# Optimization experiments

Hardware: AMD Instinct MI355X
Metric: run time of the kernel (lower is better)

## Reference

```python
import jax, jax.numpy as jnp
import numpy as np

N_NODES = 100000
N_EDGES = 1600000
IN_F = 128
OUT_F = 64
BN_EPS = 1e-5


def setup_inputs() -> dict:
    key = jax.random.key(0)
    ks = jax.random.split(key, 6)
    feature = jax.random.normal(ks[0], (N_NODES, IN_F), dtype=jnp.float32)
    src = jax.random.randint(ks[1], (N_EDGES,), 0, N_NODES, dtype=jnp.int32)
    dst = jax.random.randint(ks[2], (N_EDGES,), 0, N_NODES, dtype=jnp.int32)
    W = jax.random.normal(ks[3], (IN_F, OUT_F), dtype=jnp.float32) * 0.05
    b = jnp.zeros((OUT_F,), dtype=jnp.float32)
    res_W = jax.random.normal(ks[4], (IN_F, OUT_F), dtype=jnp.float32) * 0.05
    res_b = jnp.zeros((OUT_F,), dtype=jnp.float32)
    gamma = jnp.ones((OUT_F,), dtype=jnp.float32)
    beta = jnp.zeros((OUT_F,), dtype=jnp.float32)
    return {"feature": feature, "src": src, "dst": dst, "W": W, "b": b,
            "res_W": res_W, "res_b": res_b, "gamma": gamma, "beta": beta,
            "idx": 0}


def _gcn_layer(feature, src, dst, W, b, res_W, res_b, gamma, beta):
    n = feature.shape[0]
    ones = jnp.ones_like(src, dtype=feature.dtype)
    # DGL norm='both': src-side uses out-degree, dst-side uses in-degree,
    # degrees clamped to min 1 (allow_zero_in_degree=True).
    out_deg = jax.ops.segment_sum(ones, src, num_segments=n)
    in_deg = jax.ops.segment_sum(ones, dst, num_segments=n)
    norm_src = jax.lax.rsqrt(jnp.maximum(out_deg, 1.0))  # [N]
    norm_dst = jax.lax.rsqrt(jnp.maximum(in_deg, 1.0))   # [N]

    # in_feats (128) > out_feats (64): DGL multiplies by W before aggregation.
    h = (feature * norm_src[:, None]) @ W                 # [N, OUT_F]
    agg = jax.ops.segment_sum(h[src], dst, num_segments=n)  # [N, OUT_F]
    conv = jax.nn.relu(agg * norm_dst[:, None] + b)

    # residual connection: activation(Linear(feature))
    res = jax.nn.relu(feature @ res_W + res_b)
    y = conv + res

    # BatchNorm1d (training mode, biased variance)
    mean = jnp.mean(y, axis=0)
    var = jnp.mean(jnp.square(y - mean), axis=0)
    y = (y - mean) * jax.lax.rsqrt(var + BN_EPS) * gamma + beta
    return y


def reference(feature, src, dst, W, b, res_W, res_b, gamma, beta, idx):
    # idx == 0 -> dropout branch is skipped (eval-deterministic reference)
    return _gcn_layer(feature, src, dst, W, b, res_W, res_b, gamma, beta)
```

## Files before the change

kernel.cpp:

```cpp
#include <hip/hip_runtime.h>
#include <hip/hip_fp16.h>

#define NCOL 64
#define KDIM 128
#define NB 512
#define CH 2048

typedef short bf16x8 __attribute__((ext_vector_type(8)));
typedef float f32x4 __attribute__((ext_vector_type(4)));
typedef float f32x2 __attribute__((ext_vector_type(2)));

__device__ __forceinline__ unsigned short f2bf(float f) {
    unsigned int u = __float_as_uint(f);
    return (unsigned short)((u + 0x7fffu + ((u >> 16) & 1u)) >> 16);
}

__global__ __launch_bounds__(256) void coarse_hist(const int* __restrict__ src,
                                                   const int* __restrict__ dst,
                                                   int* __restrict__ outcnt,
                                                   int* __restrict__ bcnt, int E) {
    __shared__ int lh[NB];
    int tid = threadIdx.x;
    for (int i = tid; i < NB; i += 256) lh[i] = 0;
    __syncthreads();
    int i = blockIdx.x * blockDim.x + tid;
    int stride = gridDim.x * blockDim.x;
    for (int e = i; e < E; e += stride) {
        atomicAdd(&outcnt[src[e]], 1);
        atomicAdd(&lh[dst[e] >> 8], 1);
    }
    __syncthreads();
    for (int k = tid; k < NB; k += 256) {
        int c = lh[k];
        if (c) atomicAdd(&bcnt[k], c);
    }
}

__global__ __launch_bounds__(256) void bucket_scan(const int* __restrict__ bcnt,
                                                   int* __restrict__ bbase, int* __restrict__ bcur,
                                                   int* __restrict__ row_start, int N, int E) {
    __shared__ int wsum[8];
    int tid = threadIdx.x, lane = tid & 63, wv = tid >> 6;
    int a = bcnt[tid], b = bcnt[tid + 256];
    int ia = a, ib = b;
#pragma unroll
    for (int off = 1; off < 64; off <<= 1) {
        int t = __shfl_up(ia, off); if (lane >= off) ia += t;
        int u = __shfl_up(ib, off); if (lane >= off) ib += u;
    }
    if (lane == 63) { wsum[wv] = ia; wsum[4 + wv] = ib; }
    __syncthreads();
    if (tid == 0) { int run = 0; for (int i = 0; i < 8; ++i) { int t = wsum[i]; wsum[i] = run; run += t; } }
    __syncthreads();
    int ea = wsum[wv] + ia - a;
    int eb = wsum[4 + wv] + ib - b;
    bbase[tid] = ea; bcur[tid] = ea;
    bbase[tid + 256] = eb; bcur[tid + 256] = eb;
    if (tid == 0) row_start[N] = E;
}

__global__ __launch_bounds__(256) void partition_kernel(
    const int* __restrict__ src, const int* __restrict__ dst,
    int* __restrict__ bcur, uint2* __restrict__ pairs, int E) {
    __shared__ int hist[NB];
    __shared__ int lbase[NB];
    __shared__ int gbase[NB];
    __shared__ int lcur[NB];
    __shared__ uint2 sp[CH];
    __shared__ int wsum[8];

    int tid = threadIdx.x, lane = tid & 63, wv = tid >> 6;
    int c0 = blockIdx.x * CH;
    int cnt = min(CH, E - c0);

    for (int i = tid; i < NB; i += 256) hist[i] = 0;
    __syncthreads();
    for (int i = tid; i < cnt; i += 256)
        atomicAdd(&hist[dst[c0 + i] >> 8], 1);
    __syncthreads();

    {
        int a = hist[tid], b = hist[tid + 256];
        int ia = a, ib = b;
#pragma unroll
        for (int off = 1; off < 64; off <<= 1) {
            int t = __shfl_up(ia, off); if (lane >= off) ia += t;
            int u = __shfl_up(ib, off); if (lane >= off) ib += u;
        }
        if (lane == 63) { wsum[wv] = ia; wsum[4 + wv] = ib; }
        __syncthreads();
        if (tid == 0) { int run = 0; for (int i = 0; i < 8; ++i) { int t = wsum[i]; wsum[i] = run; run += t; } }
        __syncthreads();
        lbase[tid] = wsum[wv] + ia - a;
        lbase[tid + 256] = wsum[4 + wv] + ib - b;
    }
    __syncthreads();

    for (int k = tid; k < NB; k += 256) {
        int c = hist[k];
        gbase[k] = c ? atomicAdd(&bcur[k], c) : 0;
        lcur[k] = lbase[k];
    }
    __syncthreads();

    for (int i = tid; i < cnt; i += 256) {
        int s = src[c0 + i], d = dst[c0 + i];
        int p = atomicAdd(&lcur[d >> 8], 1);
        sp[p] = make_uint2((unsigned)s, (unsigned)d);
    }
    __syncthreads();

    for (int i = tid; i < cnt; i += 256) {
        uint2 p = sp[i];
        int k = (int)(p.y >> 8);
        pairs[gbase[k] + (i - lbase[k])] = p;
    }
}

__global__ __launch_bounds__(256) void fine_kernel(
    const uint2* __restrict__ pairs, const int* __restrict__ bbase,
    int* __restrict__ row_start, int* __restrict__ ssrc, int E, int nbuck, int N) {
    __shared__ int hist[256];
    __shared__ int cur[256];
    __shared__ int wsum[4];
    int k = blockIdx.x;
    int tid = threadIdx.x, lane = tid & 63, wv = tid >> 6;
    int b0 = bbase[k];
    int b1 = (k + 1 < nbuck) ? bbase[k + 1] : E;

    hist[tid] = 0;
    __syncthreads();
    for (int i = b0 + tid; i < b1; i += 256)
        atomicAdd(&hist[pairs[i].y & 255], 1);
    __syncthreads();

    int x = hist[tid], inc = x;
#pragma unroll
    for (int off = 1; off < 64; off <<= 1) {
        int t = __shfl_up(inc, off); if (lane >= off) inc += t;
    }
    if (lane == 63) wsum[wv] = inc;
    __syncthreads();
    if (tid == 0) { int run = 0; for (int i = 0; i < 4; ++i) { int t = wsum[i]; wsum[i] = run; run += t; } }
    __syncthreads();
    int excl = wsum[wv] + inc - x;

    int d = (k << 8) + tid;
    if (d < N) row_start[d] = b0 + excl;
    cur[tid] = b0 + excl;
    __syncthreads();

    for (int i = b0 + tid; i < b1; i += 256) {
        uint2 p = pairs[i];
        int pos = atomicAdd(&cur[p.y & 255], 1);
        ssrc[pos] = (int)p.x;
    }
}

__global__ __launch_bounds__(256) void matmul_mfma(
    const float* __restrict__ feat, const float* __restrict__ W,
    const float* __restrict__ RW, const float* __restrict__ res_b,
    const int* __restrict__ outcnt,
    unsigned int* __restrict__ hb8, float* __restrict__ y, int N) {
    __shared__ bf16x8 Bf[2048];
    int tid = threadIdx.x;
    for (int idx = tid; idx < 2048; idx += 256) {
        int mat = idx >> 10;
        int kc = (idx >> 8) & 3;
        int ct = (idx >> 6) & 3;
        int l = idx & 63;
        const float* Wp = mat ? RW : W;
        int kbase = kc * 32 + (l >> 4) * 8;
        int col = ct * 16 + (l & 15);
        bf16x8 t;
#pragma unroll
        for (int j = 0; j < 8; ++j)
            t[j] = (short)f2bf(Wp[(size_t)(kbase + j) * NCOL + col]);
        Bf[idx] = t;
    }
    __syncthreads();

    int lane = tid & 63;
    int wid = tid >> 6;
    int wave = blockIdx.x * 4 + wid;
    int nwaves = gridDim.x * 4;
    int ntiles = (N + 15) >> 4;
    int c16 = lane & 15, kg = lane >> 4;

    float rbv[4];
#pragma unroll
    for (int ct = 0; ct < 4; ++ct) rbv[ct] = res_b[ct * 16 + c16];

    for (int tile = wave; tile < ntiles; tile += nwaves) {
        int tb = tile << 4;
        f32x4 acch[4], accr[4];
#pragma unroll
        for (int ct = 0; ct < 4; ++ct) {
            acch[ct] = (f32x4){0.f, 0.f, 0.f, 0.f};
            accr[ct] = (f32x4){0.f, 0.f, 0.f, 0.f};
        }

        int arow = tb + c16; if (arow >= N) arow = N - 1;
        const float* fp = feat + (size_t)arow * KDIM + kg * 8;
#pragma unroll
        for (int kc = 0; kc < 4; ++kc) {
            float4 a0 = *(const float4*)(fp + kc * 32);
            float4 a1 = *(const float4*)(fp + kc * 32 + 4);
            bf16x8 af;
            af[0] = (short)f2bf(a0.x); af[1] = (short)f2bf(a0.y);
            af[2] = (short)f2bf(a0.z); af[3] = (short)f2bf(a0.w);
            af[4] = (short)f2bf(a1.x); af[5] = (short)f2bf(a1.y);
            af[6] = (short)f2bf(a1.z); af[7] = (short)f2bf(a1.w);
#pragma unroll
            for (int ct = 0; ct < 4; ++ct) {
                acch[ct] = __builtin_amdgcn_mfma_f32_16x16x32_bf16(
                    af, Bf[(kc * 4 + ct) * 64 + lane], acch[ct], 0, 0, 0);
                accr[ct] = __builtin_amdgcn_mfma_f32_16x16x32_bf16(
                    af, Bf[1024 + (kc * 4 + ct) * 64 + lane], accr[ct], 0, 0, 0);
            }
        }

        float nrm[4];
#pragma unroll
        for (int r = 0; r < 4; ++r) {
            int rw = tb + kg * 4 + r; if (rw >= N) rw = N - 1;
            nrm[r] = rsqrtf(fmaxf((float)outcnt[rw], 1.0f));
        }
#pragma unroll
        for (int r = 0; r < 4; ++r) {
            int row = tb + kg * 4 + r;
            if (row < N) {
                unsigned int p = 0;
                p = (unsigned int)__builtin_amdgcn_cvt_pk_fp8_f32(
                        acch[0][r] * nrm[r], acch[1][r] * nrm[r], (int)p, false);
                p = (unsigned int)__builtin_amdgcn_cvt_pk_fp8_f32(
                        acch[2][r] * nrm[r], acch[3][r] * nrm[r], (int)p, true);
#pragma unroll
                for (int ct = 0; ct < 4; ++ct)
                    y[(size_t)row * NCOL + ct * 16 + c16] = fmaxf(accr[ct][r] + rbv[ct], 0.0f);
                hb8[(size_t)row * 16 + c16] = p;
            }
        }
    }
}

#define GATHER_ROW_STEP(eBase, eEnd, A0, A1, A2, A3)                                   \
    {                                                                                   \
        int e0 = (eBase) + e4, e1 = e0 + 4;                                             \
        int i0 = (e0 < (eEnd)) ? ssrc[e0] : -1;                                         \
        int i1 = (e1 < (eEnd)) ? ssrc[e1] : -1;                                         \
        unsigned int v0 = (i0 >= 0) ? hb8[(size_t)i0 * 16 + dw] : 0u;                   \
        unsigned int v1 = (i1 >= 0) ? hb8[(size_t)i1 * 16 + dw] : 0u;                   \
        f32x2 l0 = __builtin_amdgcn_cvt_pk_f32_fp8((int)v0, false);                     \
        f32x2 h0 = __builtin_amdgcn_cvt_pk_f32_fp8((int)v0, true);                      \
        f32x2 l1 = __builtin_amdgcn_cvt_pk_f32_fp8((int)v1, false);                     \
        f32x2 h1 = __builtin_amdgcn_cvt_pk_f32_fp8((int)v1, true);                      \
        A0 += l0[0] + l1[0]; A1 += l0[1] + l1[1];                                       \
        A2 += h0[0] + h1[0]; A3 += h0[1] + h1[1];                                       \
    }

__global__ __launch_bounds__(256) void gather_kernel(
    const int* __restrict__ row_start, const int* __restrict__ ssrc,
    const unsigned int* __restrict__ hb8, const float* __restrict__ b,
    float* __restrict__ y, float* __restrict__ stats, int N) {
    int tid = threadIdx.x, lane = tid & 63, wid = tid >> 6;
    int e4 = lane >> 4, dw = lane & 15;
    int rowSel = e4 >> 1;
    int colLo = ((e4 & 1) << 5) + dw;
    int wave = blockIdx.x * 4 + wid;
    int nwaves = gridDim.x * 4;

    float bcLo = b[colLo], bcHi = b[colLo + 16];
    float bnLo = 0.f, bnHi = 0.f, bnsqLo = 0.f, bnsqHi = 0.f;

    for (int d0 = wave * 2; d0 < N; d0 += 2 * nwaves) {
        int d1 = d0 + 1;
        int a0 = row_start[d0], a1 = row_start[d0 + 1];
        int b0e = 0, b1e = 0;
        if (d1 < N) { b0e = a1; b1e = row_start[d1 + 1]; }

        float A0 = 0.f, A1 = 0.f, A2 = 0.f, A3 = 0.f;
        float B0 = 0.f, B1 = 0.f, B2 = 0.f, B3 = 0.f;
        int nit = max((a1 - a0 + 7) >> 3, (b1e - b0e + 7) >> 3);
        for (int it = 0; it < nit; ++it) {
            GATHER_ROW_STEP(a0 + it * 8, a1, A0, A1, A2, A3)
            GATHER_ROW_STEP(b0e + it * 8, b1e, B0, B1, B2, B3)
        }

#pragma unroll
        for (int off = 16; off <= 32; off <<= 1) {
            A0 += __shfl_xor(A0, off); A1 += __shfl_xor(A1, off);
            A2 += __shfl_xor(A2, off); A3 += __shfl_xor(A3, off);
            B0 += __shfl_xor(B0, off); B1 += __shfl_xor(B1, off);
            B2 += __shfl_xor(B2, off); B3 += __shfl_xor(B3, off);
        }

        int dd = d0 + rowSel;
        if (dd < N) {
            int deg = rowSel ? (b1e - b0e) : (a1 - a0);
            float nd = rsqrtf(fmaxf((float)deg, 1.0f));
            float vLo = rowSel ? ((e4 & 1) ? B2 : B0) : ((e4 & 1) ? A2 : A0);
            float vHi = rowSel ? ((e4 & 1) ? B3 : B1) : ((e4 & 1) ? A3 : A1);
            float* yp = &y[(size_t)dd * NCOL + colLo];
            float v0 = fmaxf(vLo * nd + bcLo, 0.f) + yp[0];
            float v1 = fmaxf(vHi * nd + bcHi, 0.f) + yp[16];
            yp[0] = v0;
            yp[16] = v1;
            bnLo += v0; bnsqLo += v0 * v0;
            bnHi += v1; bnsqHi += v1 * v1;
        }
    }

    bnLo += __shfl_xor(bnLo, 32); bnsqLo += __shfl_xor(bnsqLo, 32);
    bnHi += __shfl_xor(bnHi, 32); bnsqHi += __shfl_xor(bnsqHi, 32);

    __shared__ float bnred[4][128];
    if (lane < 32) {
        bnred[wid][colLo] = bnLo;
        bnred[wid][colLo + 16] = bnHi;
        bnred[wid][64 + colLo] = bnsqLo;
        bnred[wid][64 + colLo + 16] = bnsqHi;
    }
    __syncthreads();
    if (tid < 128) {
        float v = bnred[0][tid] + bnred[1][tid] + bnred[2][tid] + bnred[3][tid];
        unsafeAtomicAdd(&stats[tid], v);
    }
}

__global__ void bnparam_kernel(const float* __restrict__ gamma, const float* __restrict__ beta,
                               float* __restrict__ stats, float invN) {
    int c = threadIdx.x;
    float mean = stats[c] * invN;
    float var = stats[64 + c] * invN - mean * mean;
    float s = gamma[c] * rsqrtf(var + 1e-5f);
    stats[128 + c] = s;
    stats[192 + c] = beta[c] - mean * s;
}

__global__ __launch_bounds__(256) void apply_kernel(float* __restrict__ y,
                                                    const float* __restrict__ stats, int total4) {
    int i = blockIdx.x * blockDim.x + threadIdx.x;
    int stride = gridDim.x * blockDim.x;
    float4* y4 = (float4*)y;
    for (; i < total4; i += stride) {
        float4 v = y4[i];
        int cbase = (i & 15) << 2;
        float4 s = *(const float4*)&stats[128 + cbase];
        float4 t = *(const float4*)&stats[192 + cbase];
        v.x = v.x * s.x + t.x;
        v.y = v.y * s.y + t.y;
        v.z = v.z * s.z + t.z;
        v.w = v.w * s.w + t.w;
        y4[i] = v;
    }
}

extern "C" void kernel_launch(void* const* d_in, const int* in_sizes, int n_in,
                              void* d_out, int out_size, void* d_ws, size_t ws_size,
                              hipStream_t stream) {
    const float* feat  = (const float*)d_in[0];
    const int*   src   = (const int*)d_in[1];
    const int*   dst   = (const int*)d_in[2];
    const float* W     = (const float*)d_in[3];
    const float* b     = (const float*)d_in[4];
    const float* RW    = (const float*)d_in[5];
    const float* rb    = (const float*)d_in[6];
    const float* gamma = (const float*)d_in[7];
    const float* beta  = (const float*)d_in[8];

    int N = in_sizes[0] / KDIM;
    int E = in_sizes[1];
    float* out = (float*)d_out;
    int nbuck = (N + 255) >> 8;

    char* wsb = (char*)d_ws;
    unsigned int* hb8 = (unsigned int*)wsb;                wsb += (size_t)N * 16 * 4;
    uint2* pairs    = (uint2*)wsb;                         wsb += (size_t)E * 8;
    int*   ssrc     = (int*)wsb;                           wsb += (size_t)E * 4;
    int*   row_start= (int*)wsb;                           wsb += (size_t)(N + 1) * 4;
    int*   outcnt   = (int*)wsb;                           wsb += (size_t)N * 4;
    float* stats    = (float*)wsb;                         wsb += 256 * 4;
    int*   bcnt     = (int*)wsb;                           wsb += NB * 4;
    int*   bbase    = (int*)wsb;                           wsb += NB * 4;
    int*   bcur     = (int*)wsb;

    hipMemsetAsync(outcnt, 0, ((size_t)N + 256 + NB) * 4, stream);

    coarse_hist<<<1024, 256, 0, stream>>>(src, dst, outcnt, bcnt, E);
    bucket_scan<<<1, 256, 0, stream>>>(bcnt, bbase, bcur, row_start, N, E);
    matmul_mfma<<<512, 256, 0, stream>>>(feat, W, RW, rb, outcnt, hb8, out, N);
    partition_kernel<<<(E + CH - 1) / CH, 256, 0, stream>>>(src, dst, bcur, pairs, E);
    fine_kernel<<<nbuck, 256, 0, stream>>>(pairs, bbase, row_start, ssrc, E, nbuck, N);
    gather_kernel<<<2048, 256, 0, stream>>>(row_start, ssrc, hb8, b, out, stats, N);
    bnparam_kernel<<<1, 64, 0, stream>>>(gamma, beta, stats, 1.0f / (float)N);
    apply_kernel<<<2048, 256, 0, stream>>>(out, stats, (N * NCOL) / 4);
}
```

Measured before the change: 278.1 us.

## Replace full CSR sort with 128-row buckets and LDS atomic aggregation

Result: slower. 838.4 us (+201.5%).

```diff
diff --git a/kernel.cpp b/kernel.cpp
--- a/kernel.cpp
+++ b/kernel.cpp
@@ -3,8 +3,10 @@
 
 #define NCOL 64
 #define KDIM 128
-#define NB 512
+#define NBB 1024
 #define CH 2048
+#define BROWS 128
+#define AST 68
 
 typedef short bf16x8 __attribute__((ext_vector_type(8)));
 typedef float f32x4 __attribute__((ext_vector_type(4)));
@@ -19,18 +21,18 @@
                                                    const int* __restrict__ dst,
                                                    int* __restrict__ outcnt,
                                                    int* __restrict__ bcnt, int E) {
-    __shared__ int lh[NB];
+    __shared__ int lh[NBB];
     int tid = threadIdx.x;
-    for (int i = tid; i < NB; i += 256) lh[i] = 0;
+    for (int i = tid; i < NBB; i += 256) lh[i] = 0;
     __syncthreads();
     int i = blockIdx.x * blockDim.x + tid;
     int stride = gridDim.x * blockDim.x;
     for (int e = i; e < E; e += stride) {
         atomicAdd(&outcnt[src[e]], 1);
-        atomicAdd(&lh[dst[e] >> 8], 1);
-    }
-    __syncthreads();
-    for (int k = tid; k < NB; k += 256) {
+        atomicAdd(&lh[dst[e] >> 7], 1);
+    }
+    __syncthreads();
+    for (int k = tid; k < NBB; k += 256) {
         int c = lh[k];
         if (c) atomicAdd(&bcnt[k], c);
     }
@@ -38,65 +40,70 @@
 
 __global__ __launch_bounds__(256) void bucket_scan(const int* __restrict__ bcnt,
                                                    int* __restrict__ bbase, int* __restrict__ bcur,
-                                                   int* __restrict__ row_start, int N, int E) {
-    __shared__ int wsum[8];
+                                                   int E) {
+    __shared__ int wsum[4];
     int tid = threadIdx.x, lane = tid & 63, wv = tid >> 6;
-    int a = bcnt[tid], b = bcnt[tid + 256];
-    int ia = a, ib = b;
+    int4 c = *(const int4*)&bcnt[tid * 4];
+    int s = c.x + c.y + c.z + c.w;
+    int inc = s;
 #pragma unroll
     for (int off = 1; off < 64; off <<= 1) {
-        int t = __shfl_up(ia, off); if (lane >= off) ia += t;
-        int u = __shfl_up(ib, off); if (lane >= off) ib += u;
-    }
-    if (lane == 63) { wsum[wv] = ia; wsum[4 + wv] = ib; }
-    __syncthreads();
-    if (tid == 0) { int run = 0; for (int i = 0; i < 8; ++i) { int t = wsum[i]; wsum[i] = run; run += t; } }
-    __syncthreads();
-    int ea = wsum[wv] + ia - a;
-    int eb = wsum[4 + wv] + ib - b;
-    bbase[tid] = ea; bcur[tid] = ea;
-    bbase[tid + 256] = eb; bcur[tid + 256] = eb;
-    if (tid == 0) row_start[N] = E;
+        int t = __shfl_up(inc, off); if (lane >= off) inc += t;
+    }
+    if (lane == 63) wsum[wv] = inc;
+    __syncthreads();
+    if (tid == 0) { int run = 0; for (int i = 0; i < 4; ++i) { int t = wsum[i]; wsum[i] = run; run += t; } }
+    __syncthreads();
+    int excl = wsum[wv] + inc - s;
+    int b0 = excl, b1 = b0 + c.x, b2 = b1 + c.y, b3 = b2 + c.z;
+    bbase[4 * tid] = b0; bbase[4 * tid + 1] = b1;
+    bbase[4 * tid + 2] = b2; bbase[4 * tid + 3] = b3;
+    bcur[4 * tid] = b0; bcur[4 * tid + 1] = b1;
+    bcur[4 * tid + 2] = b2; bcur[4 * tid + 3] = b3;
+    if (tid == 255) bbase[NBB] = excl + s;
 }
 
 __global__ __launch_bounds__(256) void partition_kernel(
     const int* __restrict__ src, const int* __restrict__ dst,
-    int* __restrict__ bcur, uint2* __restrict__ pairs, int E) {
-    __shared__ int hist[NB];
-    __shared__ int lbase[NB];
-    __shared__ int gbase[NB];
-    __shared__ int lcur[NB];
+    int* __restrict__ bcur, unsigned int* __restrict__ pk, int E) {
+    __shared__ int hist[NBB];
+    __shared__ int lbase[NBB];
+    __shared__ int gbase[NBB];
+    __shared__ int lcur[NBB];
     __shared__ uint2 sp[CH];
-    __shared__ int wsum[8];
+    __shared__ int wsum[4];
 
     int tid = threadIdx.x, lane = tid & 63, wv = tid >> 6;
     int c0 = blockIdx.x * CH;
     int cnt = min(CH, E - c0);
 
-    for (int i = tid; i < NB; i += 256) hist[i] = 0;
+    for (int i = tid; i < NBB; i += 256) hist[i] = 0;
     __syncthreads();
     for (int i = tid; i < cnt; i += 256)
-        atomicAdd(&hist[dst[c0 + i] >> 8], 1);
+        atomicAdd(&hist[dst[c0 + i] >> 7], 1);
     __syncthreads();
 
     {
-        int a = hist[tid], b = hist[tid + 256];
-        int ia = a, ib = b;
+        int h0 = hist[4 * tid], h1 = hist[4 * tid + 1], h2 = hist[4 * tid + 2], h3 = hist[4 * tid + 3];
+        int s = h0 + h1 + h2 + h3;
+        int inc = s;
 #pragma unroll
         for (int off = 1; off < 64; off <<= 1) {
-            int t = __shfl_up(ia, off); if (lane >= off) ia += t;
-            int u = __shfl_up(ib, off); if (lane >= off) ib += u;
-        }
-        if (lane == 63) { wsum[wv] = ia; wsum[4 + wv] = ib; }
+            int t = __shfl_up(inc, off); if (lane >= off) inc += t;
+        }
+        if (lane == 63) wsum[wv] = inc;
         __syncthreads();
-        if (tid == 0) { int run = 0; for (int i = 0; i < 8; ++i) { int t = wsum[i]; wsum[i] = run; run += t; } }
+        if (tid == 0) { int run = 0; for (int i = 0; i < 4; ++i) { int t = wsum[i]; wsum[i] = run; run += t; } }
         __syncthreads();
-        lbase[tid] = wsum[wv] + ia - a;
-        lbase[tid + 256] = wsum[4 + wv] + ib - b;
-    }
-    __syncthreads();
-
-    for (int k = tid; k < NB; k += 256) {
+        int excl = wsum[wv] + inc - s;
+        lbase[4 * tid] = excl;
+        lbase[4 * tid + 1] = excl + h0;
+        lbase[4 * tid + 2] = excl + h0 + h1;
+        lbase[4 * tid + 3] = excl + h0 + h1 + h2;
+    }
+    __syncthreads();
+
+    for (int k = tid; k < NBB; k += 256) {
         int c = hist[k];
         gbase[k] = c ? atomicAdd(&bcur[k], c) : 0;
         lcur[k] = lbase[k];
@@ -105,55 +112,15 @@
 
     for (int i = tid; i < cnt; i += 256) {
         int s = src[c0 + i], d = dst[c0 + i];
-        int p = atomicAdd(&lcur[d >> 8], 1);
+        int p = atomicAdd(&lcur[d >> 7], 1);
         sp[p] = make_uint2((unsigned)s, (unsigned)d);
     }
     __syncthreads();
 
     for (int i = tid; i < cnt; i += 256) {
         uint2 p = sp[i];
-        int k = (int)(p.y >> 8);
-        pairs[gbase[k] + (i - lbase[k])] = p;
-    }
-}
-
-__global__ __launch_bounds__(256) void fine_kernel(
-    const uint2* __restrict__ pairs, const int* __restrict__ bbase,
-    int* __restrict__ row_start, int* __restrict__ ssrc, int E, int nbuck, int N) {
-    __shared__ int hist[256];
-    __shared__ int cur[256];
-    __shared__ int wsum[4];
-    int k = blockIdx.x;
-    int tid = threadIdx.x, lane = tid & 63, wv = tid >> 6;
-    int b0 = bbase[k];
-    int b1 = (k + 1 < nbuck) ? bbase[k + 1] : E;
-
-    hist[tid] = 0;
-    __syncthreads();
-    for (int i = b0 + tid; i < b1; i += 256)
-        atomicAdd(&hist[pairs[i].y & 255], 1);
-    __syncthreads();
-
-    int x = hist[tid], inc = x;
-#pragma unroll
-    for (int off = 1; off < 64; off <<= 1) {
-        int t = __shfl_up(inc, off); if (lane >= off) inc += t;
-    }
-    if (lane == 63) wsum[wv] = inc;
-    __syncthreads();
-    if (tid == 0) { int run = 0; for (int i = 0; i < 4; ++i) { int t = wsum[i]; wsum[i] = run; run += t; } }
-    __syncthreads();
-    int excl = wsum[wv] + inc - x;
-
-    int d = (k << 8) + tid;
-    if (d < N) row_start[d] = b0 + excl;
-    cur[tid] = b0 + excl;
-    __syncthreads();
-
-    for (int i = b0 + tid; i < b1; i += 256) {
-        uint2 p = pairs[i];
-        int pos = atomicAdd(&cur[p.y & 255], 1);
-        ssrc[pos] = (int)p.x;
+        int k = (int)(p.y >> 7);
+        pk[gbase[k] + (i - lbase[k])] = ((p.y & 127u) << 17) | p.x;
     }
 }
 
@@ -244,82 +211,84 @@
     }
 }
 
-#define GATHER_ROW_STEP(eBase, eEnd, A0, A1, A2, A3)                                   \
-    {                                                                                   \
-        int e0 = (eBase) + e4, e1 = e0 + 4;                                             \
-        int i0 = (e0 < (eEnd)) ? ssrc[e0] : -1;                                         \
-        int i1 = (e1 < (eEnd)) ? ssrc[e1] : -1;                                         \
-        unsigned int v0 = (i0 >= 0) ? hb8[(size_t)i0 * 16 + dw] : 0u;                   \
-        unsigned int v1 = (i1 >= 0) ? hb8[(size_t)i1 * 16 + dw] : 0u;                   \
-        f32x2 l0 = __builtin_amdgcn_cvt_pk_f32_fp8((int)v0, false);                     \
-        f32x2 h0 = __builtin_amdgcn_cvt_pk_f32_fp8((int)v0, true);                      \
-        f32x2 l1 = __builtin_amdgcn_cvt_pk_f32_fp8((int)v1, false);                     \
-        f32x2 h1 = __builtin_amdgcn_cvt_pk_f32_fp8((int)v1, true);                      \
-        A0 += l0[0] + l1[0]; A1 += l0[1] + l1[1];                                       \
-        A2 += h0[0] + h1[0]; A3 += h0[1] + h1[1];                                       \
-    }
-
-__global__ __launch_bounds__(256) void gather_kernel(
-    const int* __restrict__ row_start, const int* __restrict__ ssrc,
+__global__ __launch_bounds__(256) void gather_lds(
+    const unsigned int* __restrict__ pk, const int* __restrict__ bbase,
     const unsigned int* __restrict__ hb8, const float* __restrict__ b,
     float* __restrict__ y, float* __restrict__ stats, int N) {
+    __shared__ float acc[BROWS * AST];
+    __shared__ int cnt[BROWS];
+    __shared__ float bnred[4][128];
     int tid = threadIdx.x, lane = tid & 63, wid = tid >> 6;
     int e4 = lane >> 4, dw = lane & 15;
-    int rowSel = e4 >> 1;
-    int colLo = ((e4 & 1) << 5) + dw;
-    int wave = blockIdx.x * 4 + wid;
-    int nwaves = gridDim.x * 4;
-
-    float bcLo = b[colLo], bcHi = b[colLo + 16];
-    float bnLo = 0.f, bnHi = 0.f, bnsqLo = 0.f, bnsqHi = 0.f;
-
-    for (int d0 = wave * 2; d0 < N; d0 += 2 * nwaves) {
-        int d1 = d0 + 1;
-        int a0 = row_start[d0], a1 = row_start[d0 + 1];
-        int b0e = 0, b1e = 0;
-        if (d1 < N) { b0e = a1; b1e = row_start[d1 + 1]; }
-
-        float A0 = 0.f, A1 = 0.f, A2 = 0.f, A3 = 0.f;
-        float B0 = 0.f, B1 = 0.f, B2 = 0.f, B3 = 0.f;
-        int nit = max((a1 - a0 + 7) >> 3, (b1e - b0e + 7) >> 3);
-        for (int it = 0; it < nit; ++it) {
-            GATHER_ROW_STEP(a0 + it * 8, a1, A0, A1, A2, A3)
-            GATHER_ROW_STEP(b0e + it * 8, b1e, B0, B1, B2, B3)
-        }
-
-#pragma unroll
-        for (int off = 16; off <= 32; off <<= 1) {
-            A0 += __shfl_xor(A0, off); A1 += __shfl_xor(A1, off);
-            A2 += __shfl_xor(A2, off); A3 += __shfl_xor(A3, off);
-            B0 += __shfl_xor(B0, off); B1 += __shfl_xor(B1, off);
-            B2 += __shfl_xor(B2, off); B3 += __shfl_xor(B3, off);
-        }
-
-        int dd = d0 + rowSel;
-        if (dd < N) {
-            int deg = rowSel ? (b1e - b0e) : (a1 - a0);
-            float nd = rsqrtf(fmaxf((float)deg, 1.0f));
-            float vLo = rowSel ? ((e4 & 1) ? B2 : B0) : ((e4 & 1) ? A2 : A0);
-            float vHi = rowSel ? ((e4 & 1) ? B3 : B1) : ((e4 & 1) ? A3 : A1);
-            float* yp = &y[(size_t)dd * NCOL + colLo];
-            float v0 = fmaxf(vLo * nd + bcLo, 0.f) + yp[0];
-            float v1 = fmaxf(vHi * nd + bcHi, 0.f) + yp[16];
-            yp[0] = v0;
-            yp[16] = v1;
-            bnLo += v0; bnsqLo += v0 * v0;
-            bnHi += v1; bnsqHi += v1 * v1;
-        }
-    }
-
-    bnLo += __shfl_xor(bnLo, 32); bnsqLo += __shfl_xor(bnsqLo, 32);
-    bnHi += __shfl_xor(bnHi, 32); bnsqHi += __shfl_xor(bnsqHi, 32);
-
-    __shared__ float bnred[4][128];
-    if (lane < 32) {
-        bnred[wid][colLo] = bnLo;
-        bnred[wid][colLo + 16] = bnHi;
-        bnred[wid][64 + colLo] = bnsqLo;
-        bnred[wid][64 + colLo + 16] = bnsqHi;
+    int k = blockIdx.x;
+    int b0 = bbase[k];
+    int b1 = bbase[k + 1];
+
+    for (int i = tid; i < BROWS * AST; i += 256) acc[i] = 0.f;
+    if (tid < BROWS) cnt[tid] = 0;
+    __syncthreads();
+
+    for (int e = b0 + wid * 32; e < b1; e += 128) {
+        int eb = e + e4 * 8;
+        unsigned int p[8], v[8];
+#pragma unroll
+        for (int u = 0; u < 8; ++u) {
+            int idx = eb + u;
+            p[u] = (idx < b1) ? pk[idx] : 0xFFFFFFFFu;
+        }
+#pragma unroll
+        for (int u = 0; u < 8; ++u)
+            v[u] = (p[u] != 0xFFFFFFFFu) ? hb8[(size_t)(p[u] & 0x1FFFFu) * 16 + dw] : 0u;
+#pragma unroll
+        for (int u = 0; u < 8; ++u) {
+            if (p[u] != 0xFFFFFFFFu) {
+                int dl = (int)(p[u] >> 17);
+                f32x2 lo = __builtin_amdgcn_cvt_pk_f32_fp8((int)v[u], false);
+                f32x2 hi = __builtin_amdgcn_cvt_pk_f32_fp8((int)v[u], true);
+                float* ap = &acc[dl * AST];
+                atomicAdd(&ap[dw], lo[0]);
+                atomicAdd(&ap[16 + dw], lo[1]);
+                atomicAdd(&ap[32 + dw], hi[0]);
+                atomicAdd(&ap[48 + dw], hi[1]);
+                if (dw == 0) atomicAdd(&cnt[dl], 1);
+            }
+        }
+    }
+    __syncthreads();
+
+    int q = tid & 15;
+    int dst0 = k << 7;
+    float4 bc = *(const float4*)&b[q * 4];
+    float bs0 = 0.f, bs1 = 0.f, bs2 = 0.f, bs3 = 0.f;
+    float sq0 = 0.f, sq1 = 0.f, sq2 = 0.f, sq3 = 0.f;
+    for (int i = tid; i < BROWS * 16; i += 256) {
+        int row = i >> 4;
+        int d = dst0 + row;
+        if (d < N) {
+            float nd = rsqrtf(fmaxf((float)cnt[row], 1.0f));
+            float4 a = *(const float4*)&acc[row * AST + q * 4];
+            float* yp = &y[(size_t)d * NCOL + q * 4];
+            float4 r = *(const float4*)yp;
+            float4 v;
+            v.x = fmaxf(a.x * nd + bc.x, 0.f) + r.x;
+            v.y = fmaxf(a.y * nd + bc.y, 0.f) + r.y;
+            v.z = fmaxf(a.z * nd + bc.z, 0.f) + r.z;
+            v.w = fmaxf(a.w * nd + bc.w, 0.f) + r.w;
+            *(float4*)yp = v;
+            bs0 += v.x; bs1 += v.y; bs2 += v.z; bs3 += v.w;
+            sq0 += v.x * v.x; sq1 += v.y * v.y; sq2 += v.z * v.z; sq3 += v.w * v.w;
+        }
+    }
+#pragma unroll
+    for (int off = 16; off <= 32; off <<= 1) {
+        bs0 += __shfl_xor(bs0, off); bs1 += __shfl_xor(bs1, off);
+        bs2 += __shfl_xor(bs2, off); bs3 += __shfl_xor(bs3, off);
+        sq0 += __shfl_xor(sq0, off); sq1 += __shfl_xor(sq1, off);
+        sq2 += __shfl_xor(sq2, off); sq3 += __shfl_xor(sq3, off);
+    }
+    if (lane < 16) {
+        *(float4*)&bnred[wid][q * 4] = make_float4(bs0, bs1, bs2, bs3);
+        *(float4*)&bnred[wid][64 + q * 4] = make_float4(sq0, sq1, sq2, sq3);
     }
     __syncthreads();
     if (tid < 128) {
@@ -372,27 +341,24 @@
     int N = in_sizes[0] / KDIM;
     int E = in_sizes[1];
     float* out = (float*)d_out;
-    int nbuck = (N + 255) >> 8;
+    int nbuck = (N + BROWS - 1) >> 7;
 
     char* wsb = (char*)d_ws;
     unsigned int* hb8 = (unsigned int*)wsb;                wsb += (size_t)N * 16 * 4;
-    uint2* pairs    = (uint2*)wsb;                         wsb += (size_t)E * 8;
-    int*   ssrc     = (int*)wsb;                           wsb += (size_t)E * 4;
-    int*   row_start= (int*)wsb;                           wsb += (size_t)(N + 1) * 4;
+    unsigned int* pk  = (unsigned int*)wsb;                wsb += (size_t)E * 4;
     int*   outcnt   = (int*)wsb;                           wsb += (size_t)N * 4;
     float* stats    = (float*)wsb;                         wsb += 256 * 4;
-    int*   bcnt     = (int*)wsb;                           wsb += NB * 4;
-    int*   bbase    = (int*)wsb;                           wsb += NB * 4;
+    int*   bcnt     = (int*)wsb;                           wsb += NBB * 4;
+    int*   bbase    = (int*)wsb;                           wsb += (NBB + 1) * 4;
     int*   bcur     = (int*)wsb;
 
-    hipMemsetAsync(outcnt, 0, ((size_t)N + 256 + NB) * 4, stream);
-
-    coarse_hist<<<1024, 256, 0, stream>>>(src, dst, outcnt, bcnt, E);
-    bucket_scan<<<1, 256, 0, stream>>>(bcnt, bbase, bcur, row_start, N, E);
+    hipMemsetAsync(outcnt, 0, ((size_t)N + 256 + NBB) * 4, stream);
+
+    coarse_hist<<<512, 256, 0, stream>>>(src, dst, outcnt, bcnt, E);
+    bucket_scan<<<1, 256, 0, stream>>>(bcnt, bbase, bcur, E);
     matmul_mfma<<<512, 256, 0, stream>>>(feat, W, RW, rb, outcnt, hb8, out, N);
-    partition_kernel<<<(E + CH - 1) / CH, 256, 0, stream>>>(src, dst, bcur, pairs, E);
-    fine_kernel<<<nbuck, 256, 0, stream>>>(pairs, bbase, row_start, ssrc, E, nbuck, N);
-    gather_kernel<<<2048, 256, 0, stream>>>(row_start, ssrc, hb8, b, out, stats, N);
+    partition_kernel<<<(E + CH - 1) / CH, 256, 0, stream>>>(src, dst, bcur, pk, E);
+    gather_lds<<<nbuck, 256, 0, stream>>>(pk, bbase, hb8, b, out, stats, N);
     bnparam_kernel<<<1, 64, 0, stream>>>(gamma, beta, stats, 1.0f / (float)N);
     apply_kernel<<<2048, 256, 0, stream>>>(out, stats, (N * NCOL) / 4);
 }
```
